# Kernel optimization log

Hardware: AMD Instinct MI355X
Metric: run time of the kernel (lower is better)

Reference implementation:

```python
import jax, jax.numpy as jnp
import numpy as np

N = 50000        # nodes
E = 1600000      # edges
D_IN = 128       # input feature size
H = 4            # attention heads
C = 16           # hidden_size1 (per-head out channels)
HC = H * C       # 64
HS2 = 64         # hidden_size2
EDGE_DIM = 4
EPS = 1e-5


def setup_inputs() -> dict:
    key = jax.random.key(0)
    ks = jax.random.split(key, 64)
    inp = {}
    inp["data_x"] = jax.random.normal(ks[0], (N, D_IN), jnp.float32)
    inp["data_edge_index"] = jax.random.randint(ks[1], (2, E), 0, N)
    inp["data_edge_attr"] = jax.random.normal(ks[2], (E, EDGE_DIM), jnp.float32)
    i = 3
    s = 0.1
    for l, din in enumerate([D_IN, HC]):
        inp[f"Wl{l}"] = jax.random.normal(ks[i], (din, HC), jnp.float32) * s; i += 1
        inp[f"bl{l}"] = jnp.zeros((HC,), jnp.float32)
        inp[f"Wr{l}"] = jax.random.normal(ks[i], (din, HC), jnp.float32) * s; i += 1
        inp[f"br{l}"] = jnp.zeros((HC,), jnp.float32)
        inp[f"We{l}"] = jax.random.normal(ks[i], (EDGE_DIM, HC), jnp.float32) * s; i += 1
        inp[f"att{l}"] = jax.random.normal(ks[i], (H, C), jnp.float32) * s; i += 1
        inp[f"bias{l}"] = jnp.zeros((HC,), jnp.float32)
        inp[f"g{l}"] = jnp.ones((HC,), jnp.float32)
        inp[f"be{l}"] = jnp.zeros((HC,), jnp.float32)
    inp["W1"] = jax.random.normal(ks[i], (HC, HS2), jnp.float32) * s; i += 1
    inp["b1"] = jnp.zeros((HS2,), jnp.float32)
    inp["gf"] = jnp.ones((HS2,), jnp.float32)
    inp["bf"] = jnp.zeros((HS2,), jnp.float32)
    inp["W2"] = jax.random.normal(ks[i], (HS2, 1), jnp.float32) * s; i += 1
    inp["b2"] = jnp.zeros((1,), jnp.float32)
    return inp


def batch_norm(x, g, b):
    mu = x.mean(0)
    var = x.var(0)  # biased variance, matching torch BN normalization
    return (x - mu) * jax.lax.rsqrt(var + EPS) * g + b


def gatv2_layer(x, src, dst, eattr, Wl, bl, Wr, br, We, att, bias):
    # GATv2Conv, add_self_loops=False, concat=True, negative_slope=0.2
    n = x.shape[0]
    xl = (x @ Wl + bl).reshape(n, H, C)   # source transform (x_j side)
    xr = (x @ Wr + br).reshape(n, H, C)   # destination transform (x_i side)
    e = (eattr @ We).reshape(-1, H, C)    # edge-feature transform
    m = xl[src] + xr[dst] + e             # [E,H,C]
    m = jnp.where(m > 0, m, 0.2 * m)      # LeakyReLU(0.2)
    a = jnp.einsum('ehc,hc->eh', m, att)  # attention logits [E,H]
    amax = jax.ops.segment_max(a, dst, num_segments=n)   # per-dst max
    a = jnp.exp(a - amax[dst])
    asum = jax.ops.segment_sum(a, dst, num_segments=n)
    alpha = a / (asum[dst] + 1e-16)       # per-destination softmax
    out = jax.ops.segment_sum(xl[src] * alpha[:, :, None], dst, num_segments=n)
    return out.reshape(n, HC) + bias


def reference(data_x, data_edge_index, data_edge_attr,
              Wl0, bl0, Wr0, br0, We0, att0, bias0, g0, be0,
              Wl1, bl1, Wr1, br1, We1, att1, bias1, g1, be1,
              W1, b1, gf, bf, W2, b2):
    src = data_edge_index[0]
    dst = data_edge_index[1]
    layers = [(Wl0, bl0, Wr0, br0, We0, att0, bias0, g0, be0),
              (Wl1, bl1, Wr1, br1, We1, att1, bias1, g1, be1)]
    x = data_x
    for (Wl, bl, Wr, br, We, att, bias, g, be) in layers:
        x = gatv2_layer(x, src, dst, data_edge_attr, Wl, bl, Wr, br, We, att, bias)
        x = jax.nn.elu(batch_norm(x, g, be))
    x = x @ W1 + b1
    x = jax.nn.elu(batch_norm(x, gf, bf))
    return 5.0 * jnp.tanh(x @ W2 + b2)
```

## Files before the change

### kernel.cpp

```cpp
#include <hip/hip_runtime.h>
#include <hip/hip_bf16.h>
#include <cmath>

#define HC 64
typedef __hip_bfloat16 bf16;
typedef unsigned int uint;
typedef float v4f __attribute__((ext_vector_type(4)));

__device__ __forceinline__ uint pack_bf2(float a, float b) {
    __hip_bfloat162 h = __float22bfloat162_rn(make_float2(a, b));
    return *reinterpret_cast<uint*>(&h);
}
__device__ __forceinline__ float bfl(uint u) { return __uint_as_float(u << 16); }
__device__ __forceinline__ float bfh(uint u) { return __uint_as_float(u & 0xffff0000u); }


__global__ __launch_bounds__(1024) void histA_k(const int* __restrict__ dst,
                                                int* __restrict__ hist, int E, int nbk, int nblk) {
    __shared__ int lh[512];
    int t = threadIdx.x;
    for (int i = t; i < nbk; i += 1024) lh[i] = 0;
    __syncthreads();
    int base = blockIdx.x * 8192;
#pragma unroll
    for (int k = 0; k < 8; ++k) {
        int e = base + k * 1024 + t;
        if (e < E) atomicAdd(&lh[dst[e] >> 7], 1);
    }
    __syncthreads();
    for (int i = t; i < nbk; i += 1024) hist[(size_t)i * nblk + blockIdx.x] = lh[i];
}


__global__ __launch_bounds__(256) void scanB_k(int* __restrict__ hist, int* __restrict__ btot,
                                               int nblk) {
    __shared__ int tmp[256];
    __shared__ int carry;
    int b = blockIdx.x, t = threadIdx.x;
    int* row = hist + (size_t)b * nblk;
    if (t == 0) carry = 0;
    __syncthreads();
    for (int base = 0; base < nblk; base += 256) {
        int i = base + t;
        int v = (i < nblk) ? row[i] : 0;
        tmp[t] = v;
        __syncthreads();
        for (int off = 1; off < 256; off <<= 1) {
            int a = (t >= off) ? tmp[t - off] : 0;
            __syncthreads();
            tmp[t] += a;
            __syncthreads();
        }
        if (i < nblk) row[i] = carry + tmp[t] - v;
        __syncthreads();
        if (t == 0) carry += tmp[255];
        __syncthreads();
    }
    if (t == 0) btot[b] = carry;
}


__global__ __launch_bounds__(512) void scanC_k(const int* __restrict__ btot,
                                               int* __restrict__ bstart, int nbk, int E) {
    __shared__ int tmp[512];
    int t = threadIdx.x;
    int v = (t < nbk) ? btot[t] : 0;
    tmp[t] = v;
    __syncthreads();
    for (int off = 1; off < 512; off <<= 1) {
        int a = (t >= off) ? tmp[t - off] : 0;
        __syncthreads();
        tmp[t] += a;
        __syncthreads();
    }
    if (t < nbk) bstart[t] = tmp[t] - v;
    if (t == 0) bstart[nbk] = E;
}


__global__ __launch_bounds__(1024) void bucketC_k(
        const int* __restrict__ src, const int* __restrict__ dst,
        const float4* __restrict__ eattr, const int* __restrict__ hist,
        const int* __restrict__ bstart,
        uint* __restrict__ tsd, uint2* __restrict__ tea, int E, int nbk, int nblk) {
    __shared__ int lcnt[512];
    __shared__ int lbase[512];
    int t = threadIdx.x;
    for (int i = t; i < nbk; i += 1024) lcnt[i] = 0;
    __syncthreads();
    int base = blockIdx.x * 8192;
    int myd[8], mylp[8];
#pragma unroll
    for (int k = 0; k < 8; ++k) {
        int e = base + k * 1024 + t;
        if (e < E) {
            int d = dst[e];
            myd[k] = d;
            mylp[k] = atomicAdd(&lcnt[d >> 7], 1);
        } else myd[k] = -1;
    }
    __syncthreads();
    for (int i = t; i < nbk; i += 1024)
        lbase[i] = hist[(size_t)i * nblk + blockIdx.x] + bstart[i];
    __syncthreads();
#pragma unroll
    for (int k = 0; k < 8; ++k) {
        int e = base + k * 1024 + t;
        if (e >= E) continue;
        int d = myd[k];
        int pos = lbase[d >> 7] + mylp[k];
        tsd[pos] = (uint)src[e] | ((uint)(d & 127) << 25);
        float4 ea = eattr[e];
        tea[pos] = make_uint2(pack_bf2(ea.x, ea.y), pack_bf2(ea.z, ea.w));
    }
}


__global__ __launch_bounds__(256) void bucket_sort_k(
        const uint* __restrict__ tsd, const uint2* __restrict__ tea,
        const int* __restrict__ bstart,
        uint* __restrict__ spre_sorted, uint2* __restrict__ eat_sorted,
        int* __restrict__ row_start, int n) {
    __shared__ int cnt[128], pfx[128], cur[128];
    int b = blockIdx.x, t = threadIdx.x;
    int i0 = bstart[b], i1 = bstart[b + 1];
    int node0 = b << 7;
    if (t < 128) cnt[t] = 0;
    __syncthreads();
    for (int i = i0 + t; i < i1; i += 256) atomicAdd(&cnt[tsd[i] >> 25], 1);
    __syncthreads();
    if (t < 128) pfx[t] = cnt[t];
    __syncthreads();
    for (int off = 1; off < 128; off <<= 1) {
        int a = (t < 128 && t >= off) ? pfx[t - off] : 0;
        __syncthreads();
        if (t < 128) pfx[t] += a;
        __syncthreads();
    }
    if (t < 128) {
        int ex = pfx[t] - cnt[t];
        cur[t] = ex;
        if (node0 + t <= n) row_start[node0 + t] = i0 + ex;
    }
    __syncthreads();
    for (int i = i0 + t; i < i1; i += 256) {
        uint u = tsd[i];
        int dl = (int)(u >> 25);
        int pos = i0 + atomicAdd(&cur[dl], 1);
        spre_sorted[pos] = (u & 0x1FFFFFFu) << 7;
        eat_sorted[pos] = tea[i];
    }
}


__global__ __launch_bounds__(256) void lin128_k(
        const float* __restrict__ x, int n,
        const float* __restrict__ Wl, const float* __restrict__ bl,
        const float* __restrict__ Wr, const float* __restrict__ br,
        bf16* __restrict__ xl, bf16* __restrict__ xr, int ngroups16) {
    __shared__ uint sWl2[64 * 64];
    __shared__ uint sWr2[64 * 64];
    __shared__ float sx[16 * 128];
    int t = threadIdx.x;
    for (int i = t; i < 64 * 64; i += 256) {
        int k2 = i >> 6, c = i & 63;
        sWl2[i] = pack_bf2(Wl[(2 * k2) * 64 + c], Wl[(2 * k2 + 1) * 64 + c]);
        sWr2[i] = pack_bf2(Wr[(2 * k2) * 64 + c], Wr[(2 * k2 + 1) * 64 + c]);
    }
    int c = t & 63, w = t >> 6;
    float blc = bl[c], brc = br[c];
    for (int gidx = blockIdx.x; gidx < ngroups16; gidx += gridDim.x) {
        int node0 = gidx * 16;
        __syncthreads();
        for (int i = t; i < 16 * 128; i += 256) {
            int r = node0 + (i >> 7);
            sx[i] = (r < n) ? x[(size_t)r * 128 + (i & 127)] : 0.f;
        }
        __syncthreads();
        float al0 = blc, al1 = blc, al2 = blc, al3 = blc;
        float ar0 = brc, ar1 = brc, ar2 = brc, ar3 = brc;
        const float* sx0 = sx + w * 4 * 128;
#pragma unroll 8
        for (int k2 = 0; k2 < 64; ++k2) {
            uint wlu = sWl2[k2 * 64 + c], wru = sWr2[k2 * 64 + c];
            float wlx = bfl(wlu), wly = bfh(wlu);
            float wrx = bfl(wru), wry = bfh(wru);
            float2 xa = *(const float2*)&sx0[k2 * 2];
            float2 xb = *(const float2*)&sx0[128 + k2 * 2];
            float2 xc = *(const float2*)&sx0[256 + k2 * 2];
            float2 xd = *(const float2*)&sx0[384 + k2 * 2];
            al0 = fmaf(xa.x, wlx, al0); al0 = fmaf(xa.y, wly, al0);
            ar0 = fmaf(xa.x, wrx, ar0); ar0 = fmaf(xa.y, wry, ar0);
            al1 = fmaf(xb.x, wlx, al1); al1 = fmaf(xb.y, wly, al1);
            ar1 = fmaf(xb.x, wrx, ar1); ar1 = fmaf(xb.y, wry, ar1);
            al2 = fmaf(xc.x, wlx, al2); al2 = fmaf(xc.y, wly, al2);
            ar2 = fmaf(xc.x, wrx, ar2); ar2 = fmaf(xc.y, wry, ar2);
            al3 = fmaf(xd.x, wlx, al3); al3 = fmaf(xd.y, wly, al3);
            ar3 = fmaf(xd.x, wrx, ar3); ar3 = fmaf(xd.y, wry, ar3);
        }
        int nb_ = node0 + w * 4;
        if (nb_ + 0 < n) { xl[(size_t)(nb_ + 0) * 64 + c] = __float2bfloat16(al0); xr[(size_t)(nb_ + 0) * 64 + c] = __float2bfloat16(ar0); }
        if (nb_ + 1 < n) { xl[(size_t)(nb_ + 1) * 64 + c] = __float2bfloat16(al1); xr[(size_t)(nb_ + 1) * 64 + c] = __float2bfloat16(ar1); }
        if (nb_ + 2 < n) { xl[(size_t)(nb_ + 2) * 64 + c] = __float2bfloat16(al2); xr[(size_t)(nb_ + 2) * 64 + c] = __float2bfloat16(ar2); }
        if (nb_ + 3 < n) { xl[(size_t)(nb_ + 3) * 64 + c] = __float2bfloat16(al3); xr[(size_t)(nb_ + 3) * 64 + c] = __float2bfloat16(ar3); }
    }
}


__global__ __launch_bounds__(256) void lin64bn_k(
        const float* __restrict__ x, int n,
        const float* __restrict__ sums, const float* __restrict__ sqs,
        const float* __restrict__ g, const float* __restrict__ be,
        const float* __restrict__ Wl, const float* __restrict__ bl,
        const float* __restrict__ Wr, const float* __restrict__ br,
        bf16* __restrict__ xl, bf16* __restrict__ xr, int ngroups16) {
    __shared__ uint sWl2[32 * 64];
    __shared__ uint sWr2[32 * 64];
    __shared__ float sx[16 * 64];
    __shared__ float ssc[64], ssh[64];
    int t = threadIdx.x;
    if (t < 64) {
        float inv_n = 1.f / n;
        float mu = sums[t] * inv_n;
        float var = sqs[t] * inv_n - mu * mu;
        float sc = rsqrtf(var + 1e-5f) * g[t];
        ssc[t] = sc; ssh[t] = be[t] - mu * sc;
    }
    for (int i = t; i < 32 * 64; i += 256) {
        int k2 = i >> 6, c = i & 63;
        sWl2[i] = pack_bf2(Wl[(2 * k2) * 64 + c], Wl[(2 * k2 + 1) * 64 + c]);
        sWr2[i] = pack_bf2(Wr[(2 * k2) * 64 + c], Wr[(2 * k2 + 1) * 64 + c]);
    }
    int c = t & 63, w = t >> 6;
    float blc = bl[c], brc = br[c];
    for (int gidx = blockIdx.x; gidx < ngroups16; gidx += gridDim.x) {
        int node0 = gidx * 16;
        __syncthreads();
        for (int i = t; i < 16 * 64; i += 256) {
            int r = node0 + (i >> 6);
            float v = (r < n) ? x[(size_t)r * 64 + (i & 63)] : 0.f;
            v = v * ssc[i & 63] + ssh[i & 63];
            sx[i] = v > 0.f ? v : __expf(v) - 1.f;
        }
        __syncthreads();
        float al0 = blc, al1 = blc, al2 = blc, al3 = blc;
        float ar0 = brc, ar1 = brc, ar2 = brc, ar3 = brc;
        const float* sx0 = sx + w * 4 * 64;
#pragma unroll 8
        for (int k2 = 0; k2 < 32; ++k2) {
            uint wlu = sWl2[k2 * 64 + c], wru = sWr2[k2 * 64 + c];
            float wlx = bfl(wlu), wly = bfh(wlu);
            float wrx = bfl(wru), wry = bfh(wru);
            float2 xa = *(const float2*)&sx0[k2 * 2];
            float2 xb = *(const float2*)&sx0[64 + k2 * 2];
            float2 xc = *(const float2*)&sx0[128 + k2 * 2];
            float2 xd = *(const float2*)&sx0[192 + k2 * 2];
            al0 = fmaf(xa.x, wlx, al0); al0 = fmaf(xa.y, wly, al0);
            ar0 = fmaf(xa.x, wrx, ar0); ar0 = fmaf(xa.y, wry, ar0);
            al1 = fmaf(xb.x, wlx, al1); al1 = fmaf(xb.y, wly, al1);
            ar1 = fmaf(xb.x, wrx, ar1); ar1 = fmaf(xb.y, wry, ar1);
            al2 = fmaf(xc.x, wlx, al2); al2 = fmaf(xc.y, wly, al2);
            ar2 = fmaf(xc.x, wrx, ar2); ar2 = fmaf(xc.y, wry, ar2);
            al3 = fmaf(xd.x, wlx, al3); al3 = fmaf(xd.y, wly, al3);
            ar3 = fmaf(xd.x, wrx, ar3); ar3 = fmaf(xd.y, wry, ar3);
        }
        int nb_ = node0 + w * 4;
        if (nb_ + 0 < n) { xl[(size_t)(nb_ + 0) * 64 + c] = __float2bfloat16(al0); xr[(size_t)(nb_ + 0) * 64 + c] = __float2bfloat16(ar0); }
        if (nb_ + 1 < n) { xl[(size_t)(nb_ + 1) * 64 + c] = __float2bfloat16(al1); xr[(size_t)(nb_ + 1) * 64 + c] = __float2bfloat16(ar1); }
        if (nb_ + 2 < n) { xl[(size_t)(nb_ + 2) * 64 + c] = __float2bfloat16(al2); xr[(size_t)(nb_ + 2) * 64 + c] = __float2bfloat16(ar2); }
        if (nb_ + 3 < n) { xl[(size_t)(nb_ + 3) * 64 + c] = __float2bfloat16(al3); xr[(size_t)(nb_ + 3) * 64 + c] = __float2bfloat16(ar3); }
    }
}


__global__ __launch_bounds__(256) void gat_node_k(
        const bf16* __restrict__ xl, const bf16* __restrict__ xr,
        const float* __restrict__ We, const float* __restrict__ att,
        const int* __restrict__ row_start, const uint* __restrict__ spre,
        const uint2* __restrict__ eat,
        float* __restrict__ out, int n) {
    int t = threadIdx.x;
    int lane = t & 63;
    int quad = lane >> 4;
    int c4 = lane & 15;
    int node = blockIdx.x * 4 + (t >> 6);
    if (node >= n) return;
    int c0 = c4 << 2;
    v4f w0 = {We[c0], We[c0 + 1], We[c0 + 2], We[c0 + 3]};
    v4f w1 = {We[64 + c0], We[64 + c0 + 1], We[64 + c0 + 2], We[64 + c0 + 3]};
    v4f w2 = {We[128 + c0], We[128 + c0 + 1], We[128 + c0 + 2], We[128 + c0 + 3]};
    v4f w3 = {We[192 + c0], We[192 + c0 + 1], We[192 + c0 + 2], We[192 + c0 + 3]};
    v4f ratt = {att[c0] * 1.44269504f, att[c0 + 1] * 1.44269504f,
                att[c0 + 2] * 1.44269504f, att[c0 + 3] * 1.44269504f};
    const char* xlb = (const char*)xl;
    uint2 xru = *(const uint2*)((const char*)xr + ((size_t)node << 7) + ((uint)c0 << 1));
    v4f xrd = {bfl(xru.x), bfh(xru.x), bfl(xru.y), bfh(xru.y)};
    int rs = row_start[node], re = row_start[node + 1];
    v4f acc = {0.f, 0.f, 0.f, 0.f};
    float srun = 0.f;
    uint coff = (uint)c4 << 3;

#define PROC(EA, XU) { \
        v4f xv = {bfl((XU).x), bfh((XU).x), bfl((XU).y), bfh((XU).y)}; \
        v4f z = xv + xrd; \
        float e0 = bfl((EA).x), e1 = bfh((EA).x); \
        float e2 = bfl((EA).y), e3 = bfh((EA).y); \
        z += e0 * w0; z += e1 * w1; z += e2 * w2; z += e3 * w3; \
        z = __builtin_elementwise_max(z, 0.2f * z); \
        v4f zr = z * ratt; \
        float v = (zr.x + zr.y) + (zr.z + zr.w); \
        v += __shfl_xor(v, 1); v += __shfl_xor(v, 2); \
        float p = exp2f(v); \
        srun += p; \
        acc += p * xv; \
    }

    int i = rs;
    for (; i + 16 <= re; i += 16) {
        uint sp0 = spre[i + quad],      sp1 = spre[i + 4 + quad];
        uint sp2 = spre[i + 8 + quad],  sp3 = spre[i + 12 + quad];
        uint2 ea0 = eat[i + quad],      ea1 = eat[i + 4 + quad];
        uint2 ea2 = eat[i + 8 + quad],  ea3 = eat[i + 12 + quad];
        uint2 xu0 = *(const uint2*)(xlb + sp0 + coff);
        uint2 xu1 = *(const uint2*)(xlb + sp1 + coff);
        uint2 xu2 = *(const uint2*)(xlb + sp2 + coff);
        uint2 xu3 = *(const uint2*)(xlb + sp3 + coff);
        PROC(ea0, xu0);
        PROC(ea1, xu1);
        PROC(ea2, xu2);
        PROC(ea3, xu3);
    }
    for (; i + 8 <= re; i += 8) {
        uint spA = spre[i + quad], spB = spre[i + 4 + quad];
        uint2 eaA = eat[i + quad], eaB = eat[i + 4 + quad];
        uint2 xuA = *(const uint2*)(xlb + spA + coff);
        uint2 xuB = *(const uint2*)(xlb + spB + coff);
        PROC(eaA, xuA);
        PROC(eaB, xuB);
    }
    for (; i < re; i += 4) {
        int ei = i + quad;
        bool ok = ei < re;
        int eic = ok ? ei : i;
        uint sp = spre[eic];
        uint2 ea = eat[eic];
        uint2 xu = *(const uint2*)(xlb + sp + coff);
        v4f xv = {bfl(xu.x), bfh(xu.x), bfl(xu.y), bfh(xu.y)};
        v4f z = xv + xrd;
        float e0 = bfl(ea.x), e1 = bfh(ea.x);
        float e2 = bfl(ea.y), e3 = bfh(ea.y);
        z += e0 * w0; z += e1 * w1; z += e2 * w2; z += e3 * w3;
        z = __builtin_elementwise_max(z, 0.2f * z);
        v4f zr = z * ratt;
        float v = (zr.x + zr.y) + (zr.z + zr.w);
        v += __shfl_xor(v, 1); v += __shfl_xor(v, 2);
        float p = ok ? exp2f(v) : 0.f;
        srun += p;
        acc += p * xv;
    }
#undef PROC

    srun += __shfl_xor(srun, 16);  srun += __shfl_xor(srun, 32);
    acc.x += __shfl_xor(acc.x, 16); acc.x += __shfl_xor(acc.x, 32);
    acc.y += __shfl_xor(acc.y, 16); acc.y += __shfl_xor(acc.y, 32);
    acc.z += __shfl_xor(acc.z, 16); acc.z += __shfl_xor(acc.z, 32);
    acc.w += __shfl_xor(acc.w, 16); acc.w += __shfl_xor(acc.w, 32);
    if (quad == 0) {
        float inv = 1.f / (srun + 1e-16f);
        v4f o = acc * inv;
        *(v4f*)&out[((size_t)node << 6) + (uint)c0] = o;
    }
}


__global__ void bn_stats_k(const float* __restrict__ x, float* __restrict__ sums,
                           float* __restrict__ sqs, int n) {
    __shared__ float ls[256], lq[256];
    int t = threadIdx.x;
    int c = t & 63, sub = t >> 6;
    float s = 0.f, q = 0.f;
    for (int r = blockIdx.x * 4 + sub; r < n; r += gridDim.x * 4) {
        float v = x[(size_t)r * 64 + c];
        s += v;
        q = fmaf(v, v, q);
    }
    ls[t] = s; lq[t] = q;
    __syncthreads();
    if (t < 128) { ls[t] += ls[t + 128]; lq[t] += lq[t + 128]; }
    __syncthreads();
    if (t < 64) {
        atomicAdd(&sums[c], ls[t] + ls[t + 64]);
        atomicAdd(&sqs[c], lq[t] + lq[t + 64]);
    }
}


__global__ __launch_bounds__(256) void lin1_k(
        const float* __restrict__ x, int n,
        const float* __restrict__ sums, const float* __restrict__ sqs,
        const float* __restrict__ g, const float* __restrict__ be,
        const float* __restrict__ W, const float* __restrict__ b,
        float* __restrict__ y, float* __restrict__ sums_o, float* __restrict__ sqs_o,
        int ngroups16) {
    __shared__ uint sW2[32 * 64];
    __shared__ float sx[16 * 64];
    __shared__ float ssc[64], ssh[64];
    __shared__ float ls[256], lq[256];
    int t = threadIdx.x;
    if (t < 64) {
        float inv_n = 1.f / n;
        float mu = sums[t] * inv_n;
        float var = sqs[t] * inv_n - mu * mu;
        float sc = rsqrtf(var + 1e-5f) * g[t];
        ssc[t] = sc; ssh[t] = be[t] - mu * sc;
    }
    for (int i = t; i < 32 * 64; i += 256) {
        int k2 = i >> 6, c = i & 63;
        sW2[i] = pack_bf2(W[(2 * k2) * 64 + c], W[(2 * k2 + 1) * 64 + c]);
    }
    int c = t & 63, w = t >> 6;
    float bc = b[c];
    float s = 0.f, q = 0.f;
    for (int gidx = blockIdx.x; gidx < ngroups16; gidx += gridDim.x) {
        int node0 = gidx * 16;
        __syncthreads();
        for (int i = t; i < 16 * 64; i += 256) {
            int r = node0 + (i >> 6);
            float v = (r < n) ? x[(size_t)r * 64 + (i & 63)] : 0.f;
            v = v * ssc[i & 63] + ssh[i & 63];
            sx[i] = v > 0.f ? v : __expf(v) - 1.f;
        }
        __syncthreads();
        float a0 = bc, a1 = bc, a2 = bc, a3 = bc;
        const float* sx0 = sx + w * 4 * 64;
#pragma unroll 8
        for (int k2 = 0; k2 < 32; ++k2) {
            uint wu = sW2[k2 * 64 + c];
            float wx = bfl(wu), wy = bfh(wu);
            float2 xa = *(const float2*)&sx0[k2 * 2];
            float2 xb = *(const float2*)&sx0[64 + k2 * 2];
            float2 xc = *(const float2*)&sx0[128 + k2 * 2];
            float2 xd = *(const float2*)&sx0[192 + k2 * 2];
            a0 = fmaf(xa.x, wx, a0); a0 = fmaf(xa.y, wy, a0);
            a1 = fmaf(xb.x, wx, a1); a1 = fmaf(xb.y, wy, a1);
            a2 = fmaf(xc.x, wx, a2); a2 = fmaf(xc.y, wy, a2);
            a3 = fmaf(xd.x, wx, a3); a3 = fmaf(xd.y, wy, a3);
        }
        int nb_ = node0 + w * 4;
        if (nb_ + 0 < n) { y[(size_t)(nb_ + 0) * 64 + c] = a0; s += a0; q = fmaf(a0, a0, q); }
        if (nb_ + 1 < n) { y[(size_t)(nb_ + 1) * 64 + c] = a1; s += a1; q = fmaf(a1, a1, q); }
        if (nb_ + 2 < n) { y[(size_t)(nb_ + 2) * 64 + c] = a2; s += a2; q = fmaf(a2, a2, q); }
        if (nb_ + 3 < n) { y[(size_t)(nb_ + 3) * 64 + c] = a3; s += a3; q = fmaf(a3, a3, q); }
    }
    __syncthreads();
    ls[t] = s; lq[t] = q;
    __syncthreads();
    if (t < 64) {
        float ss = ls[t] + ls[t + 64] + ls[t + 128] + ls[t + 192];
        float qq = lq[t] + lq[t + 64] + lq[t + 128] + lq[t + 192];
        atomicAdd(&sums_o[t], ss);
        atomicAdd(&sqs_o[t], qq);
    }
}


__global__ void final_k(const float* __restrict__ z, int n,
                        const float* __restrict__ sums, const float* __restrict__ sqs,
                        const float* __restrict__ g, const float* __restrict__ be,
                        const float* __restrict__ W2, const float* __restrict__ b2,
                        float* __restrict__ out) {
    int t = blockIdx.x * blockDim.x + threadIdx.x;
    int node = t >> 6, c = t & 63;
    if (node >= n) return;
    float inv_n = 1.f / n;
    float mu = sums[c] * inv_n;
    float var = sqs[c] * inv_n - mu * mu;
    float scc = rsqrtf(var + 1e-5f) * g[c];
    float sh = be[c] - mu * scc;
    float v = z[(size_t)node * 64 + c] * scc + sh;
    v = v > 0.f ? v : __expf(v) - 1.f;
    v *= W2[c];
    v += __shfl_xor(v, 1);
    v += __shfl_xor(v, 2);
    v += __shfl_xor(v, 4);
    v += __shfl_xor(v, 8);
    v += __shfl_xor(v, 16);
    v += __shfl_xor(v, 32);
    if (c == 0) out[node] = 5.0f * tanhf(v + b2[0]);
}


extern "C" void kernel_launch(void* const* d_in, const int* in_sizes, int n_in,
                              void* d_out, int out_size, void* d_ws, size_t ws_size,
                              hipStream_t stream) {
    const float* x0    = (const float*)d_in[0];
    const int*   eidx  = (const int*)d_in[1];
    const float* eattr = (const float*)d_in[2];

    const float* Wl[2]; const float* bl[2]; const float* Wr[2]; const float* br[2];
    const float* We[2]; const float* att[2]; const float* g[2]; const float* be[2];
    for (int l = 0; l < 2; ++l) {
        int base = 3 + l * 9;
        Wl[l]  = (const float*)d_in[base + 0];
        bl[l]  = (const float*)d_in[base + 1];
        Wr[l]  = (const float*)d_in[base + 2];
        br[l]  = (const float*)d_in[base + 3];
        We[l]  = (const float*)d_in[base + 4];
        att[l] = (const float*)d_in[base + 5];
        g[l]   = (const float*)d_in[base + 7];
        be[l]  = (const float*)d_in[base + 8];
    }
    const float* W1 = (const float*)d_in[21];
    const float* b1 = (const float*)d_in[22];
    const float* gf = (const float*)d_in[23];
    const float* bf = (const float*)d_in[24];
    const float* W2 = (const float*)d_in[25];
    const float* b2 = (const float*)d_in[26];

    const int N = in_sizes[0] / 128;
    const int E = in_sizes[1] / 2;
    const int* src = eidx;
    const int* dst = eidx + E;
    const int nbk = (N + 127) >> 7;
    const int nblkA = (E + 8191) / 8192;

    float* ws = (float*)d_ws;
    size_t o = 0;
    float* regionA = ws + o; o += (size_t)2 * N * HC;
    uint2* tea = (uint2*)regionA;
    uint*  tsd = (uint*)(regionA + (size_t)2 * E);
    float* h0  = regionA;
    float* h1  = regionA + (size_t)N * HC;
    uint2* eat_sorted = (uint2*)(ws + o); o += (size_t)E * 2;
    uint*  spre_sorted = (uint*)(ws + o);  o += (size_t)E;
    bf16*  xl  = (bf16*)(ws + o);  o += (size_t)N * 32;
    bf16*  xr  = (bf16*)(ws + o);  o += (size_t)N * 32;
    int*   row_start = (int*)(ws + o); o += (size_t)N + 1;
    int*   hist   = (int*)(ws + o); o += (size_t)nbk * nblkA + 64;
    float* stats  = ws + o; o += 6 * HC;
    int*   bstart = (int*)(ws + o); o += 513;
    int*   btot   = (int*)(ws + o); o += 512;
    float* s0 = stats,        *q0 = stats + 64;
    float* s1 = stats + 128,  *q1 = stats + 192;
    float* sf = stats + 256,  *qf = stats + 320;

    const int ngroups4  = (N + 3) / 4;
    const int ngroups16 = (N + 15) / 16;
    const int lin_grid = ngroups16 < 1024 ? ngroups16 : 1024;

    hipMemsetAsync(stats, 0, 6 * HC * 4, stream);

    histA_k<<<nblkA, 1024, 0, stream>>>(dst, hist, E, nbk, nblkA);
    scanB_k<<<nbk, 256, 0, stream>>>(hist, btot, nblkA);
    scanC_k<<<1, 512, 0, stream>>>(btot, bstart, nbk, E);
    bucketC_k<<<nblkA, 1024, 0, stream>>>(src, dst, (const float4*)eattr, hist, bstart,
                                          tsd, tea, E, nbk, nblkA);
    bucket_sort_k<<<nbk, 256, 0, stream>>>(tsd, tea, bstart, spre_sorted, eat_sorted,
                                           row_start, N);

    lin128_k<<<lin_grid, 256, 0, stream>>>(x0, N, Wl[0], bl[0], Wr[0], br[0], xl, xr, ngroups16);
    gat_node_k<<<ngroups4, 256, 0, stream>>>(xl, xr, We[0], att[0], row_start,
                                             spre_sorted, eat_sorted, h0, N);
    bn_stats_k<<<256, 256, 0, stream>>>(h0, s0, q0, N);

    lin64bn_k<<<lin_grid, 256, 0, stream>>>(h0, N, s0, q0, g[0], be[0],
                                            Wl[1], bl[1], Wr[1], br[1], xl, xr, ngroups16);
    gat_node_k<<<ngroups4, 256, 0, stream>>>(xl, xr, We[1], att[1], row_start,
                                             spre_sorted, eat_sorted, h1, N);
    bn_stats_k<<<256, 256, 0, stream>>>(h1, s1, q1, N);

    float* y = h0;
    lin1_k<<<lin_grid, 256, 0, stream>>>(h1, N, s1, q1, g[1], be[1], W1, b1, y, sf, qf, ngroups16);
    final_k<<<(int)(((size_t)N * 64 + 255) / 256), 256, 0, stream>>>(
        y, N, sf, qf, gf, bf, W2, b2, (float*)d_out);
}
```

Baseline: 354.5 us.

## Fuse BN statistics into GAT aggregation and use packed float2 FMAs in linears

Removes the separate bn_stats kernel by accumulating per-channel sum and sum-of-squares inside gat_node_k. Each block reduces through shared-memory atomics, then issues one global atomic per channel. This avoids a re-read of the 50000x64 layer output and one launch per layer, at the cost of extra atomics and keeping out-of-range waves alive until a barrier. Separately, the linear kernels now accumulate in two-wide vectors (v2f) so the compiler can emit packed FMA instructions, with bias added after the loop. That changes the summation order slightly.

```diff
diff --git a/kernel.cpp b/kernel.cpp
--- a/kernel.cpp
+++ b/kernel.cpp
@@ -6,6 +6,7 @@
 typedef __hip_bfloat16 bf16;
 typedef unsigned int uint;
 typedef float v4f __attribute__((ext_vector_type(4)));
+typedef float v2f __attribute__((ext_vector_type(2)));
 
 __device__ __forceinline__ uint pack_bf2(float a, float b) {
     __hip_bfloat162 h = __float22bfloat162_rn(make_float2(a, b));
@@ -177,32 +178,28 @@
             sx[i] = (r < n) ? x[(size_t)r * 128 + (i & 127)] : 0.f;
         }
         __syncthreads();
-        float al0 = blc, al1 = blc, al2 = blc, al3 = blc;
-        float ar0 = brc, ar1 = brc, ar2 = brc, ar3 = brc;
+        v2f al0 = {0.f, 0.f}, al1 = al0, al2 = al0, al3 = al0;
+        v2f ar0 = al0, ar1 = al0, ar2 = al0, ar3 = al0;
         const float* sx0 = sx + w * 4 * 128;
 #pragma unroll 8
         for (int k2 = 0; k2 < 64; ++k2) {
             uint wlu = sWl2[k2 * 64 + c], wru = sWr2[k2 * 64 + c];
-            float wlx = bfl(wlu), wly = bfh(wlu);
-            float wrx = bfl(wru), wry = bfh(wru);
-            float2 xa = *(const float2*)&sx0[k2 * 2];
-            float2 xb = *(const float2*)&sx0[128 + k2 * 2];
-            float2 xc = *(const float2*)&sx0[256 + k2 * 2];
-            float2 xd = *(const float2*)&sx0[384 + k2 * 2];
-            al0 = fmaf(xa.x, wlx, al0); al0 = fmaf(xa.y, wly, al0);
-            ar0 = fmaf(xa.x, wrx, ar0); ar0 = fmaf(xa.y, wry, ar0);
-            al1 = fmaf(xb.x, wlx, al1); al1 = fmaf(xb.y, wly, al1);
-            ar1 = fmaf(xb.x, wrx, ar1); ar1 = fmaf(xb.y, wry, ar1);
-            al2 = fmaf(xc.x, wlx, al2); al2 = fmaf(xc.y, wly, al2);
-            ar2 = fmaf(xc.x, wrx, ar2); ar2 = fmaf(xc.y, wry, ar2);
-            al3 = fmaf(xd.x, wlx, al3); al3 = fmaf(xd.y, wly, al3);
-            ar3 = fmaf(xd.x, wrx, ar3); ar3 = fmaf(xd.y, wry, ar3);
+            v2f wl = {bfl(wlu), bfh(wlu)};
+            v2f wr = {bfl(wru), bfh(wru)};
+            v2f xa = *(const v2f*)&sx0[k2 * 2];
+            v2f xb = *(const v2f*)&sx0[128 + k2 * 2];
+            v2f xc = *(const v2f*)&sx0[256 + k2 * 2];
+            v2f xd = *(const v2f*)&sx0[384 + k2 * 2];
+            al0 += xa * wl; ar0 += xa * wr;
+            al1 += xb * wl; ar1 += xb * wr;
+            al2 += xc * wl; ar2 += xc * wr;
+            al3 += xd * wl; ar3 += xd * wr;
         }
         int nb_ = node0 + w * 4;
-        if (nb_ + 0 < n) { xl[(size_t)(nb_ + 0) * 64 + c] = __float2bfloat16(al0); xr[(size_t)(nb_ + 0) * 64 + c] = __float2bfloat16(ar0); }
-        if (nb_ + 1 < n) { xl[(size_t)(nb_ + 1) * 64 + c] = __float2bfloat16(al1); xr[(size_t)(nb_ + 1) * 64 + c] = __float2bfloat16(ar1); }
-        if (nb_ + 2 < n) { xl[(size_t)(nb_ + 2) * 64 + c] = __float2bfloat16(al2); xr[(size_t)(nb_ + 2) * 64 + c] = __float2bfloat16(ar2); }
-        if (nb_ + 3 < n) { xl[(size_t)(nb_ + 3) * 64 + c] = __float2bfloat16(al3); xr[(size_t)(nb_ + 3) * 64 + c] = __float2bfloat16(ar3); }
+        if (nb_ + 0 < n) { xl[(size_t)(nb_ + 0) * 64 + c] = __float2bfloat16(al0.x + al0.y + blc); xr[(size_t)(nb_ + 0) * 64 + c] = __float2bfloat16(ar0.x + ar0.y + brc); }
+        if (nb_ + 1 < n) { xl[(size_t)(nb_ + 1) * 64 + c] = __float2bfloat16(al1.x + al1.y + blc); xr[(size_t)(nb_ + 1) * 64 + c] = __float2bfloat16(ar1.x + ar1.y + brc); }
+        if (nb_ + 2 < n) { xl[(size_t)(nb_ + 2) * 64 + c] = __float2bfloat16(al2.x + al2.y + blc); xr[(size_t)(nb_ + 2) * 64 + c] = __float2bfloat16(ar2.x + ar2.y + brc); }
+        if (nb_ + 3 < n) { xl[(size_t)(nb_ + 3) * 64 + c] = __float2bfloat16(al3.x + al3.y + blc); xr[(size_t)(nb_ + 3) * 64 + c] = __float2bfloat16(ar3.x + ar3.y + brc); }
     }
 }
 
@@ -243,32 +240,28 @@
             sx[i] = v > 0.f ? v : __expf(v) - 1.f;
         }
         __syncthreads();
-        float al0 = blc, al1 = blc, al2 = blc, al3 = blc;
-        float ar0 = brc, ar1 = brc, ar2 = brc, ar3 = brc;
+        v2f al0 = {0.f, 0.f}, al1 = al0, al2 = al0, al3 = al0;
+        v2f ar0 = al0, ar1 = al0, ar2 = al0, ar3 = al0;
         const float* sx0 = sx + w * 4 * 64;
 #pragma unroll 8
         for (int k2 = 0; k2 < 32; ++k2) {
             uint wlu = sWl2[k2 * 64 + c], wru = sWr2[k2 * 64 + c];
-            float wlx = bfl(wlu), wly = bfh(wlu);
-            float wrx = bfl(wru), wry = bfh(wru);
-            float2 xa = *(const float2*)&sx0[k2 * 2];
-            float2 xb = *(const float2*)&sx0[64 + k2 * 2];
-            float2 xc = *(const float2*)&sx0[128 + k2 * 2];
-            float2 xd = *(const float2*)&sx0[192 + k2 * 2];
-            al0 = fmaf(xa.x, wlx, al0); al0 = fmaf(xa.y, wly, al0);
-            ar0 = fmaf(xa.x, wrx, ar0); ar0 = fmaf(xa.y, wry, ar0);
-            al1 = fmaf(xb.x, wlx, al1); al1 = fmaf(xb.y, wly, al1);
-            ar1 = fmaf(xb.x, wrx, ar1); ar1 = fmaf(xb.y, wry, ar1);
-            al2 = fmaf(xc.x, wlx, al2); al2 = fmaf(xc.y, wly, al2);
-            ar2 = fmaf(xc.x, wrx, ar2); ar2 = fmaf(xc.y, wry, ar2);
-            al3 = fmaf(xd.x, wlx, al3); al3 = fmaf(xd.y, wly, al3);
-            ar3 = fmaf(xd.x, wrx, ar3); ar3 = fmaf(xd.y, wry, ar3);
+            v2f wl = {bfl(wlu), bfh(wlu)};
+            v2f wr = {bfl(wru), bfh(wru)};
+            v2f xa = *(const v2f*)&sx0[k2 * 2];
+            v2f xb = *(const v2f*)&sx0[64 + k2 * 2];
+            v2f xc = *(const v2f*)&sx0[128 + k2 * 2];
+            v2f xd = *(const v2f*)&sx0[192 + k2 * 2];
+            al0 += xa * wl; ar0 += xa * wr;
+            al1 += xb * wl; ar1 += xb * wr;
+            al2 += xc * wl; ar2 += xc * wr;
+            al3 += xd * wl; ar3 += xd * wr;
         }
         int nb_ = node0 + w * 4;
-        if (nb_ + 0 < n) { xl[(size_t)(nb_ + 0) * 64 + c] = __float2bfloat16(al0); xr[(size_t)(nb_ + 0) * 64 + c] = __float2bfloat16(ar0); }
-        if (nb_ + 1 < n) { xl[(size_t)(nb_ + 1) * 64 + c] = __float2bfloat16(al1); xr[(size_t)(nb_ + 1) * 64 + c] = __float2bfloat16(ar1); }
-        if (nb_ + 2 < n) { xl[(size_t)(nb_ + 2) * 64 + c] = __float2bfloat16(al2); xr[(size_t)(nb_ + 2) * 64 + c] = __float2bfloat16(ar2); }
-        if (nb_ + 3 < n) { xl[(size_t)(nb_ + 3) * 64 + c] = __float2bfloat16(al3); xr[(size_t)(nb_ + 3) * 64 + c] = __float2bfloat16(ar3); }
+        if (nb_ + 0 < n) { xl[(size_t)(nb_ + 0) * 64 + c] = __float2bfloat16(al0.x + al0.y + blc); xr[(size_t)(nb_ + 0) * 64 + c] = __float2bfloat16(ar0.x + ar0.y + brc); }
+        if (nb_ + 1 < n) { xl[(size_t)(nb_ + 1) * 64 + c] = __float2bfloat16(al1.x + al1.y + blc); xr[(size_t)(nb_ + 1) * 64 + c] = __float2bfloat16(ar1.x + ar1.y + brc); }
+        if (nb_ + 2 < n) { xl[(size_t)(nb_ + 2) * 64 + c] = __float2bfloat16(al2.x + al2.y + blc); xr[(size_t)(nb_ + 2) * 64 + c] = __float2bfloat16(ar2.x + ar2.y + brc); }
+        if (nb_ + 3 < n) { xl[(size_t)(nb_ + 3) * 64 + c] = __float2bfloat16(al3.x + al3.y + blc); xr[(size_t)(nb_ + 3) * 64 + c] = __float2bfloat16(ar3.x + ar3.y + brc); }
     }
 }
 
@@ -278,13 +271,17 @@
         const float* __restrict__ We, const float* __restrict__ att,
         const int* __restrict__ row_start, const uint* __restrict__ spre,
         const uint2* __restrict__ eat,
-        float* __restrict__ out, int n) {
-    int t = threadIdx.x;
+        float* __restrict__ out, float* __restrict__ sums, float* __restrict__ sqs, int n) {
+    __shared__ float lsum[64], lsq[64];
+    int t = threadIdx.x;
+    if (t < 64) { lsum[t] = 0.f; lsq[t] = 0.f; }
+    __syncthreads();
     int lane = t & 63;
     int quad = lane >> 4;
     int c4 = lane & 15;
     int node = blockIdx.x * 4 + (t >> 6);
-    if (node >= n) return;
+    bool valid = node < n;
+    int nclamp = valid ? node : (n - 1);
     int c0 = c4 << 2;
     v4f w0 = {We[c0], We[c0 + 1], We[c0 + 2], We[c0 + 3]};
     v4f w1 = {We[64 + c0], We[64 + c0 + 1], We[64 + c0 + 2], We[64 + c0 + 3]};
@@ -293,9 +290,10 @@
     v4f ratt = {att[c0] * 1.44269504f, att[c0 + 1] * 1.44269504f,
                 att[c0 + 2] * 1.44269504f, att[c0 + 3] * 1.44269504f};
     const char* xlb = (const char*)xl;
-    uint2 xru = *(const uint2*)((const char*)xr + ((size_t)node << 7) + ((uint)c0 << 1));
+    uint2 xru = *(const uint2*)((const char*)xr + ((size_t)nclamp << 7) + ((uint)c0 << 1));
     v4f xrd = {bfl(xru.x), bfh(xru.x), bfl(xru.y), bfh(xru.y)};
-    int rs = row_start[node], re = row_start[node + 1];
+    int rs = valid ? row_start[node] : 0;
+    int re = valid ? row_start[node + 1] : 0;
     v4f acc = {0.f, 0.f, 0.f, 0.f};
     float srun = 0.f;
     uint coff = (uint)c4 << 3;
@@ -365,32 +363,19 @@
     acc.y += __shfl_xor(acc.y, 16); acc.y += __shfl_xor(acc.y, 32);
     acc.z += __shfl_xor(acc.z, 16); acc.z += __shfl_xor(acc.z, 32);
     acc.w += __shfl_xor(acc.w, 16); acc.w += __shfl_xor(acc.w, 32);
-    if (quad == 0) {
+    if (valid && quad == 0) {
         float inv = 1.f / (srun + 1e-16f);
         v4f o = acc * inv;
         *(v4f*)&out[((size_t)node << 6) + (uint)c0] = o;
-    }
-}
-
-
-__global__ void bn_stats_k(const float* __restrict__ x, float* __restrict__ sums,
-                           float* __restrict__ sqs, int n) {
-    __shared__ float ls[256], lq[256];
-    int t = threadIdx.x;
-    int c = t & 63, sub = t >> 6;
-    float s = 0.f, q = 0.f;
-    for (int r = blockIdx.x * 4 + sub; r < n; r += gridDim.x * 4) {
-        float v = x[(size_t)r * 64 + c];
-        s += v;
-        q = fmaf(v, v, q);
-    }
-    ls[t] = s; lq[t] = q;
-    __syncthreads();
-    if (t < 128) { ls[t] += ls[t + 128]; lq[t] += lq[t + 128]; }
+        atomicAdd(&lsum[c0 + 0], o.x); atomicAdd(&lsq[c0 + 0], o.x * o.x);
+        atomicAdd(&lsum[c0 + 1], o.y); atomicAdd(&lsq[c0 + 1], o.y * o.y);
+        atomicAdd(&lsum[c0 + 2], o.z); atomicAdd(&lsq[c0 + 2], o.z * o.z);
+        atomicAdd(&lsum[c0 + 3], o.w); atomicAdd(&lsq[c0 + 3], o.w * o.w);
+    }
     __syncthreads();
     if (t < 64) {
-        atomicAdd(&sums[c], ls[t] + ls[t + 64]);
-        atomicAdd(&sqs[c], lq[t] + lq[t + 64]);
+        atomicAdd(&sums[t], lsum[t]);
+        atomicAdd(&sqs[t], lsq[t]);
     }
 }
 
@@ -431,26 +416,28 @@
             sx[i] = v > 0.f ? v : __expf(v) - 1.f;
         }
         __syncthreads();
-        float a0 = bc, a1 = bc, a2 = bc, a3 = bc;
+        v2f a0 = {0.f, 0.f}, a1 = a0, a2 = a0, a3 = a0;
         const float* sx0 = sx + w * 4 * 64;
 #pragma unroll 8
         for (int k2 = 0; k2 < 32; ++k2) {
             uint wu = sW2[k2 * 64 + c];
-            float wx = bfl(wu), wy = bfh(wu);
-            float2 xa = *(const float2*)&sx0[k2 * 2];
-            float2 xb = *(const float2*)&sx0[64 + k2 * 2];
-            float2 xc = *(const float2*)&sx0[128 + k2 * 2];
-            float2 xd = *(const float2*)&sx0[192 + k2 * 2];
-            a0 = fmaf(xa.x, wx, a0); a0 = fmaf(xa.y, wy, a0);
-            a1 = fmaf(xb.x, wx, a1); a1 = fmaf(xb.y, wy, a1);
-            a2 = fmaf(xc.x, wx, a2); a2 = fmaf(xc.y, wy, a2);
-            a3 = fmaf(xd.x, wx, a3); a3 = fmaf(xd.y, wy, a3);
+            v2f wv = {bfl(wu), bfh(wu)};
+            v2f xa = *(const v2f*)&sx0[k2 * 2];
+            v2f xb = *(const v2f*)&sx0[64 + k2 * 2];
+            v2f xc = *(const v2f*)&sx0[128 + k2 * 2];
+            v2f xd = *(const v2f*)&sx0[192 + k2 * 2];
+            a0 += xa * wv;
+            a1 += xb * wv;
+            a2 += xc * wv;
+            a3 += xd * wv;
         }
         int nb_ = node0 + w * 4;
-        if (nb_ + 0 < n) { y[(size_t)(nb_ + 0) * 64 + c] = a0; s += a0; q = fmaf(a0, a0, q); }
-        if (nb_ + 1 < n) { y[(size_t)(nb_ + 1) * 64 + c] = a1; s += a1; q = fmaf(a1, a1, q); }
-        if (nb_ + 2 < n) { y[(size_t)(nb_ + 2) * 64 + c] = a2; s += a2; q = fmaf(a2, a2, q); }
-        if (nb_ + 3 < n) { y[(size_t)(nb_ + 3) * 64 + c] = a3; s += a3; q = fmaf(a3, a3, q); }
+        float o0 = a0.x + a0.y + bc, o1 = a1.x + a1.y + bc;
+        float o2 = a2.x + a2.y + bc, o3 = a3.x + a3.y + bc;
+        if (nb_ + 0 < n) { y[(size_t)(nb_ + 0) * 64 + c] = o0; s += o0; q = fmaf(o0, o0, q); }
+        if (nb_ + 1 < n) { y[(size_t)(nb_ + 1) * 64 + c] = o1; s += o1; q = fmaf(o1, o1, q); }
+        if (nb_ + 2 < n) { y[(size_t)(nb_ + 2) * 64 + c] = o2; s += o2; q = fmaf(o2, o2, q); }
+        if (nb_ + 3 < n) { y[(size_t)(nb_ + 3) * 64 + c] = o3; s += o3; q = fmaf(o3, o3, q); }
     }
     __syncthreads();
     ls[t] = s; lq[t] = q;
@@ -560,14 +547,12 @@
 
     lin128_k<<<lin_grid, 256, 0, stream>>>(x0, N, Wl[0], bl[0], Wr[0], br[0], xl, xr, ngroups16);
     gat_node_k<<<ngroups4, 256, 0, stream>>>(xl, xr, We[0], att[0], row_start,
-                                             spre_sorted, eat_sorted, h0, N);
-    bn_stats_k<<<256, 256, 0, stream>>>(h0, s0, q0, N);
+                                             spre_sorted, eat_sorted, h0, s0, q0, N);
 
     lin64bn_k<<<lin_grid, 256, 0, stream>>>(h0, N, s0, q0, g[0], be[0],
                                             Wl[1], bl[1], Wr[1], br[1], xl, xr, ngroups16);
     gat_node_k<<<ngroups4, 256, 0, stream>>>(xl, xr, We[1], att[1], row_start,
-                                             spre_sorted, eat_sorted, h1, N);
-    bn_stats_k<<<256, 256, 0, stream>>>(h1, s1, q1, N);
+                                             spre_sorted, eat_sorted, h1, s1, q1, N);
 
     float* y = h0;
     lin1_k<<<lin_grid, 256, 0, stream>>>(h1, N, s1, q1, g[1], be[1], W1, b1, y, sf, qf, ngroups16);
```

New measurement: 1.009 ms. +184.7%, slower.
